# Optimization experiments

Measured on AMD Instinct MI355X. Metric: run time of the kernel, lower is better.

## Reference

```python
import jax, jax.numpy as jnp
import numpy as np

EMBED = 896
HQ = 16      # query heads
HK = 4       # kv heads
D = EMBED // HQ          # 56 head dim
KV_EMBED = D * HK        # 224
G = HQ // HK             # 4 groups per kv head
LN_EPS = 1e-5


def setup_inputs() -> dict:
    key = jax.random.key(0)
    ks = jax.random.split(key, 8)
    b, n = 2, 2048
    inp = {
        "query": jax.random.normal(ks[0], (b, n, EMBED), jnp.float32),
        "key":   jax.random.normal(ks[1], (b, n, EMBED), jnp.float32),
        "value": jax.random.normal(ks[2], (b, n, EMBED), jnp.float32),
        # torch Linear weights are (out_features, in_features), y = x @ W.T
        "Wq": jax.random.normal(ks[3], (EMBED, EMBED), jnp.float32) * 0.02,
        "Wk": jax.random.normal(ks[4], (KV_EMBED, EMBED), jnp.float32) * 0.02,
        "Wv": jax.random.normal(ks[5], (KV_EMBED, EMBED), jnp.float32) * 0.02,
        "Wo": jax.random.normal(ks[6], (EMBED, EMBED), jnp.float32) * 0.02,
        "ln_gamma": jnp.ones((EMBED,), jnp.float32),
        "ln_beta": jnp.zeros((EMBED,), jnp.float32),
    }
    return inp


def _layer_norm(x, gamma, beta):
    mu = jnp.mean(x, axis=-1, keepdims=True)
    var = jnp.var(x, axis=-1, keepdims=True)
    return (x - mu) * jax.lax.rsqrt(var + LN_EPS) * gamma + beta


def reference(query, key, value, Wq, Wk, Wv, Wo, ln_gamma, ln_beta):
    b, n, _ = query.shape
    s = key.shape[1]
    # projections
    q = query @ Wq.T                      # (b, n, EMBED)
    k = key @ Wk.T                        # (b, s, KV_EMBED)
    v = value @ Wv.T                      # (b, s, KV_EMBED)
    # split heads: q -> (b, hk, g, n, d); k, v -> (b, hk, s, d)
    q = q.reshape(b, n, HQ, D).transpose(0, 2, 1, 3)      # (b, hq, n, d)
    q = q.reshape(b, HK, G, n, D)                          # (b, hk, g, n, d)
    k = k.reshape(b, s, HK, D).transpose(0, 2, 1, 3)       # (b, hk, s, d)
    v = v.reshape(b, s, HK, D).transpose(0, 2, 1, 3)       # (b, hk, s, d)
    # scaled scores
    scale = jnp.asarray(D, q.dtype) ** 0.5
    scores = jnp.einsum('bhgnd,bhsd->bhgns', q, k) / scale  # (b, hk, g, n, s)
    # causal mask
    mask = jnp.tril(jnp.ones((n, s), bool))                # (n, s)
    scores = jnp.where(mask, scores, jnp.asarray(-jnp.inf, scores.dtype))
    attn = jax.nn.softmax(scores, axis=-1)                 # (b, hk, g, n, s)
    # (dropout is identity in deterministic eval-mode reference)
    out = jnp.einsum('bhgns,bhsd->bhgnd', attn, v)         # (b, hk, g, n, d)
    # merge heads back: (h g) ordering matches the query split
    out = out.transpose(0, 3, 1, 2, 4).reshape(b, n, EMBED)  # b n (h g d)
    out = _layer_norm(out, ln_gamma, ln_beta)
    out = out @ Wo.T                                        # (b, n, EMBED)
    # need_weights + average_attn_weights: b h g n s -> b n s (h g), mean over n
    aw = attn.transpose(0, 3, 4, 1, 2).reshape(b, n, s, HQ).mean(axis=1)  # (b, s, hq)
    return out, aw
```

## Files before the change

### kernel.cpp

```cpp
#include <hip/hip_runtime.h>

#define B_    2
#define N_    2048
#define EMBED 896
#define HQ    16
#define HK    4
#define D_    56
#define DP    64

typedef unsigned short u16;
typedef unsigned int   u32;
typedef __attribute__((ext_vector_type(8))) short bf16x8;
typedef __attribute__((ext_vector_type(4))) short bf16x4;
typedef __attribute__((ext_vector_type(4))) float f32x4;

__device__ __forceinline__ u16 f2bf(float f) {
  u32 u = __builtin_bit_cast(u32, f);
  return (u16)((u + 0x7FFFu + ((u >> 16) & 1u)) >> 16);
}

__device__ __forceinline__ float bf2f(u16 x) {
  u32 u = (u32)x << 16;
  return __builtin_bit_cast(float, u);
}

__device__ __forceinline__ u32 cvtpk_bf16(float lo, float hi) {
  u32 r;
  asm("v_cvt_pk_bf16_f32 %0, %1, %2" : "=v"(r) : "v"(lo), "v"(hi));
  return r;
}

#define EXP2F(x) __builtin_amdgcn_exp2f(x)

__device__ __forceinline__ void gload_lds16(const u16* g, u16* l) {
  __builtin_amdgcn_global_load_lds(
      (const __attribute__((address_space(1))) void*)g,
      (__attribute__((address_space(3))) void*)l, 16, 0, 0);
}

#define QSCALE 0.19278822f

__global__ __launch_bounds__(256) void pad_zero(u16* __restrict__ Qp,
                                                u16* __restrict__ Kp,
                                                u16* __restrict__ Vt) {
  int i = blockIdx.x * 256 + threadIdx.x;
  int4 z = {0, 0, 0, 0};
  if (i < 65536) {
    *(int4*)(Qp + (size_t)i * 64 + 56) = z;
  } else if (i < 81920) {
    *(int4*)(Kp + (size_t)(i - 65536) * 64 + 56) = z;
  } else {
    int j = i - 81920;
    int bhk = j >> 11;
    int off = j & 2047;
    *(int4*)(Vt + ((size_t)bhk * 64 + 56) * 2048 + (size_t)off * 8) = z;
  }
}

#define SEG_IN  3670016u
#define SEG_WQ  802816u
#define SEG_WK  200704u

__global__ __launch_bounds__(256) void to_bf16(
    const float* __restrict__ q, const float* __restrict__ k,
    const float* __restrict__ v, const float* __restrict__ wq,
    const float* __restrict__ wk, const float* __restrict__ wv,
    const float* __restrict__ wo, u16* __restrict__ qb, u16* __restrict__ kb,
    u16* __restrict__ vb, u16* __restrict__ wqb, u16* __restrict__ wkb,
    u16* __restrict__ wvb, u16* __restrict__ wob) {
  const size_t base = (size_t)blockIdx.x * 1024 + threadIdx.x;
  float4 v4[4];
  const float* srcs[4];
  u16* dsts[4];
  size_t offs[4];
#pragma unroll
  for (int j = 0; j < 4; j++) {
    size_t e = (base + j * 256) * 4;
    const float* src;
    u16* dst;
    size_t off;
    if (e < SEG_IN)                  { src = q;  dst = qb;  off = e; }
    else if (e < 2 * (size_t)SEG_IN) { src = k;  dst = kb;  off = e - SEG_IN; }
    else if (e < 3 * (size_t)SEG_IN) { src = v;  dst = vb;  off = e - 2 * (size_t)SEG_IN; }
    else {
      size_t r = e - 3 * (size_t)SEG_IN;
      if (r < SEG_WQ)                   { src = wq; dst = wqb; off = r; }
      else if (r < SEG_WQ + SEG_WK)     { src = wk; dst = wkb; off = r - SEG_WQ; }
      else if (r < SEG_WQ + 2 * SEG_WK) { src = wv; dst = wvb; off = r - SEG_WQ - SEG_WK; }
      else                              { src = wo; dst = wob; off = r - SEG_WQ - 2 * SEG_WK; }
    }
    srcs[j] = src; dsts[j] = dst; offs[j] = off;
    v4[j] = *(const float4*)(src + off);
  }
#pragma unroll
  for (int j = 0; j < 4; j++) {
    uint2 pb;
    pb.x = cvtpk_bf16(v4[j].x, v4[j].y);
    pb.y = cvtpk_bf16(v4[j].z, v4[j].w);
    *(uint2*)(dsts[j] + offs[j]) = pb;
  }
}

#define NT_K 14

#define GEMM_CORE(APTR, WPTR)                                                  \
  for (int it = 0; it < NT_K; ++it) {                                          \
    const int k0 = it * 64;                                                    \
    {                                                                          \
      const u16* Ag = (APTR) + (size_t)m0 * EMBED + k0;                        \
      _Pragma("unroll") for (int i = 0; i < 4; i++) {                          \
        int f = i * 256 + t;                                                   \
        int r = f >> 3, s = (f & 7) ^ (r & 7);                                 \
        gload_lds16(Ag + (size_t)r * EMBED + s * 8,                            \
                    AsL + (i * 256 + fwbase) * 8);                             \
      }                                                                        \
      const u16* Wg = (WPTR) + (size_t)wn0 * EMBED + k0;                       \
      _Pragma("unroll") for (int i = 0; i < 2; i++) {                          \
        int f = i * 256 + t;                                                   \
        int r = f >> 3, s = (f & 7) ^ (r & 7);                                 \
        gload_lds16(Wg + (size_t)r * EMBED + s * 8,                            \
                    BsL + (i * 256 + fwbase) * 8);                             \
      }                                                                        \
    }                                                                          \
    __syncthreads();                  \
    _Pragma("unroll") for (int kk = 0; kk < 2; kk++) {                         \
      bf16x8 af[2], bfv[4];                                                    \
      _Pragma("unroll") for (int mf = 0; mf < 2; mf++) {                       \
        int ra = wr + mf * 16 + fr;                                            \
        af[mf] =                                                               \
            *(const bf16x8*)&AsL[ra * 64 + ((fg + kk * 4) ^ (ra & 7)) * 8];    \
      }                                                                        \
      _Pragma("unroll") for (int nf = 0; nf < 4; nf++) {                       \
        int rb = nf * 16 + fr;                                                 \
        bfv[nf] =                                                              \
            *(const bf16x8*)&BsL[rb * 64 + ((fg + kk * 4) ^ (rb & 7)) * 8];    \
      }                                                                        \
      _Pragma("unroll") for (int mf = 0; mf < 2; mf++)                         \
          _Pragma("unroll") for (int nf = 0; nf < 4; nf++)                     \
              acc[mf][nf] = __builtin_amdgcn_mfma_f32_16x16x32_bf16(           \
                  af[mf], bfv[nf], acc[mf][nf], 0, 0, 0);                      \
    }                                                                          \
    __syncthreads();        \
  }

__global__ __launch_bounds__(256) void proj_gemm(
    const u16* __restrict__ qb, const u16* __restrict__ kb,
    const u16* __restrict__ vb, const u16* __restrict__ Wqb,
    const u16* __restrict__ Wkb, const u16* __restrict__ Wvb,
    u16* __restrict__ Qp, u16* __restrict__ Kp, u16* __restrict__ Vt) {
  __shared__ __align__(16) u16 lds[12288];
  u16* AsL = lds;
  u16* BsL = lds + 8192;
  const int t = threadIdx.x;
  const int bid = blockIdx.x;
  const int lin = (bid & 7) * 88 + (bid >> 3);
  const int y = lin / 32;
  const int m0 = (lin & 31) * 128;
  int p, nt;
  if (y < 14)      { p = 0; nt = y; }
  else if (y < 18) { p = 1; nt = y - 14; }
  else             { p = 2; nt = y - 18; }
  const u16* A = p == 0 ? qb : (p == 1 ? kb : vb);
  const u16* W = p == 0 ? Wqb : (p == 1 ? Wkb : Wvb);
  const int Nproj = p == 0 ? 896 : 224;
  const int wn0 = nt * 64;

  const int w = t >> 6, lane = t & 63;
  const int fr = lane & 15, fg = lane >> 4;
  const int wr = w * 32;
  const int fwbase = t & 192;

  f32x4 acc[2][4] = {};

  GEMM_CORE(A, W)

  if (p < 2) {
#pragma unroll
    for (int nf = 0; nf < 4; nf++) {
      int col = wn0 + nf * 16 + fr;
      if (col < Nproj) {
        int hh = col / 56, d = col - hh * 56;
#pragma unroll
        for (int mf = 0; mf < 2; mf++)
#pragma unroll
          for (int r = 0; r < 4; r++) {
            int row = m0 + wr + mf * 16 + fg * 4 + r;
            int bb = row >> 11, nn = row & 2047;
            float vv = acc[mf][nf][r];
            if (p == 0)
              Qp[((size_t)((bb * 16 + hh) * 2048 + nn)) * 64 + d] =
                  f2bf(vv * QSCALE);
            else
              Kp[((size_t)((bb * 4 + hh) * 2048 + nn)) * 64 + d] = f2bf(vv);
          }
      }
    }
  } else {
    u16* Traw = lds;
#define TS(r_, c_) Traw[(r_)*136 + (c_)]
#pragma unroll
    for (int nf = 0; nf < 4; nf++)
#pragma unroll
      for (int mf = 0; mf < 2; mf++)
#pragma unroll
        for (int r = 0; r < 4; r++)
          TS(nf * 16 + fr, wr + mf * 16 + fg * 4 + r) = f2bf(acc[mf][nf][r]);
    __syncthreads();
    const int bb = m0 >> 11, n_base = m0 & 2047;
#pragma unroll
    for (int i = 0; i < 4; i++) {
      int flat = i * 256 + t;
      int dr = flat >> 4;
      int c8 = (flat & 15) * 8;
      int col = wn0 + dr;
      if (col < 224) {
        int hh = col / 56, d = col - hh * 56;
        *(int4*)(Vt + ((size_t)((bb * 4 + hh) * 64 + d)) * 2048 + n_base + c8) =
            *(int4*)&TS(dr, c8);
      }
    }
  }
}

__global__ __launch_bounds__(256) void gemm_wo(const u16* __restrict__ A,
                                               const u16* __restrict__ W,
                                               float* __restrict__ C) {
  __shared__ __align__(16) u16 lds[12288];
  u16* AsL = lds;
  u16* BsL = lds + 8192;
  const int t = threadIdx.x;
  const int m0 = blockIdx.x * 128;
  const int wn0 = blockIdx.y * 64;
  const int w = t >> 6, lane = t & 63;
  const int fr = lane & 15, fg = lane >> 4;
  const int wr = w * 32;
  const int fwbase = t & 192;

  f32x4 acc[2][4] = {};

  GEMM_CORE(A, W)

#pragma unroll
  for (int nf = 0; nf < 4; nf++) {
    int col = wn0 + nf * 16 + fr;
#pragma unroll
    for (int mf = 0; mf < 2; mf++)
#pragma unroll
      for (int r = 0; r < 4; r++) {
        int row = m0 + wr + mf * 16 + fg * 4 + r;
        C[(size_t)row * EMBED + col] = acc[mf][nf][r];
      }
  }
}

__global__ __launch_bounds__(256) void repack_qf(const u16* __restrict__ Qp,
                                                 u16* __restrict__ Qf) {
  const int tile = blockIdx.x;
  const u16* src = Qp + (size_t)tile * 4096;
  u16* dst = Qf + (size_t)tile * 4096;
  __shared__ __align__(16) u16 T[4096];
  const int t = threadIdx.x;
#pragma unroll
  for (int i = 0; i < 2; i++) {
    int f = i * 256 + t;
    int r = f >> 3, c8 = f & 7;
    *(int4*)&T[(r * 8 + (c8 ^ (r & 7))) * 8] = *(const int4*)(src + f * 8);
  }
  __syncthreads();
#pragma unroll
  for (int i = 0; i < 2; i++) {
    int f = i * 256 + t;
    int fr = f & 15, fg = (f >> 4) & 3, kk = (f >> 6) & 1, ifr = (f >> 7) & 3;
    int row = ifr * 16 + fr, c8 = (kk * 32 + fg * 8) >> 3;
    *(int4*)(dst + f * 8) = *(int4*)&T[(row * 8 + (c8 ^ (row & 7))) * 8];
  }
}

__global__ __launch_bounds__(256) void attn_fwd(const u16* __restrict__ Qp,
                                                const u16* __restrict__ Kp,
                                                const u16* __restrict__ Vt,
                                                u16* __restrict__ Op,
                                                float* __restrict__ lp) {
  const int p = blockIdx.x, hk = blockIdx.y;
  const int b = blockIdx.z >> 1, sg = blockIdx.z & 1;
  const int t = threadIdx.x, w = t >> 6, lane = t & 63;
  const int fr = lane & 15, fg = lane >> 4;
  const int h = hk * 4 + w;

  __shared__ __align__(16) u16 KVs[2][2][4096];

  const u16* Qh = Qp + (size_t)(b * HQ + h) * N_ * DP;
  const u16* Kh = Kp + (size_t)(b * HK + hk) * N_ * DP;
  const u16* Vh = Vt + (size_t)(b * HK + hk) * DP * N_;

  const int fwb = t & 192;
  const int fx = fr & 7;

#define ISSUE_KV(ntt_, buf_)                                                   \
  do {                                                                         \
    const u16* Kb = Kh + (size_t)(ntt_)*64 * DP;                               \
    const u16* Vb = Vh + (ntt_)*64;                                            \
    _Pragma("unroll") for (int i = 0; i < 2; i++) {                            \
      int f = i * 256 + t;                                                     \
      int r = f >> 3, sl = (f & 7) ^ (r & 7);                                  \
      gload_lds16(Kb + (size_t)r * DP + sl * 8,                                \
                  &KVs[buf_][0][(i * 256 + fwb) * 8]);                         \
      gload_lds16(Vb + (size_t)r * N_ + sl * 8,                                \
                  &KVs[buf_][1][(i * 256 + fwb) * 8]);                         \
    }                                                                          \
  } while (0)

  const int s0 = p, s1 = 127 - p;
  const int ntf0 = (s0 >> 2) + 1, ntf1 = (s1 >> 2) + 1;
  const int lo0 = sg ? (ntf0 >> 1) : 0, hi0 = sg ? ntf0 : (ntf0 >> 1);
  const int lo1 = sg ? (ntf1 >> 1) : 0, hi1 = sg ? ntf1 : (ntf1 >> 1);

  int bi = 0;
  if (hi0 > lo0) {
    ISSUE_KV(lo0, 0);
  } else if (hi1 > lo1) {
    ISSUE_KV(lo1, 0);
  }

  for (int half = 0; half < 2; ++half) {
    const int s = half ? s1 : s0;
    const int ntf = half ? ntf1 : ntf0;
    const int lo = half ? lo1 : lo0, hi = half ? hi1 : hi0;

    bf16x8 qf[2];
#pragma unroll
    for (int kk = 0; kk < 2; kk++)
      qf[kk] = *(const bf16x8*)(Qh + (size_t)(s * 16 + fr) * DP +
                                kk * 32 + fg * 8);

    f32x4 oacc[4] = {};
    float l_lane = 0.f;

    for (int tt = lo; tt < hi; ++tt) {
      __syncthreads();
      {
        int ntt = -1;
        if (tt + 1 < hi) ntt = tt + 1;
        else if (half == 0 && hi1 > lo1) ntt = lo1;
        if (ntt >= 0) {
          ISSUE_KV(ntt, bi ^ 1);
        }
      }

      f32x4 sacc[4] = {};
#pragma unroll
      for (int kk = 0; kk < 2; kk++) {
        bf16x8 bk[4];
#pragma unroll
        for (int jf = 0; jf < 4; jf++)
          bk[jf] = *(const bf16x8*)&KVs[bi][0][(jf * 16 + fr) * 64 +
                                               ((kk * 4 + fg) ^ fx) * 8];
#pragma unroll
        for (int jf = 0; jf < 4; jf++)
          sacc[jf] = __builtin_amdgcn_mfma_f32_16x16x32_bf16(
              bk[jf], qf[kk], sacc[jf], 0, 0, 0);
      }

      bf16x4 pa[4];
      if (tt == ntf - 1) {
        const int gi = s * 16 + fr;
#pragma unroll
        for (int jf = 0; jf < 4; jf++) {
          float pv[4];
#pragma unroll
          for (int r = 0; r < 4; r++) {
            int gj = tt * 64 + jf * 16 + fg * 4 + r;
            pv[r] = (gj <= gi) ? EXP2F(sacc[jf][r]) : 0.f;
            l_lane += pv[r];
          }
          uint2 pk = {cvtpk_bf16(pv[0], pv[1]), cvtpk_bf16(pv[2], pv[3])};
          pa[jf] = __builtin_bit_cast(bf16x4, pk);
        }
      } else {
#pragma unroll
        for (int jf = 0; jf < 4; jf++) {
          float pv[4];
#pragma unroll
          for (int r = 0; r < 4; r++) {
            pv[r] = EXP2F(sacc[jf][r]);
            l_lane += pv[r];
          }
          uint2 pk = {cvtpk_bf16(pv[0], pv[1]), cvtpk_bf16(pv[2], pv[3])};
          pa[jf] = __builtin_bit_cast(bf16x4, pk);
        }
      }

#pragma unroll
      for (int df = 0; df < 4; df++) {
        const int vrow = (df * 16 + fr) * 64;
#pragma unroll
        for (int jf = 0; jf < 4; jf++) {
          bf16x4 bv = *(const bf16x4*)&KVs[bi][1][vrow +
                                                  (((jf * 2 + (fg >> 1)) ^ fx) * 8) +
                                                  (fg & 1) * 4];
          oacc[df] = __builtin_amdgcn_mfma_f32_16x16x16bf16_1k(
              pa[jf], bv, oacc[df], 0, 0, 0);
        }
      }
      bi ^= 1;
    }

    {
      float v = l_lane;
      v += __shfl_xor(v, 16);
      v += __shfl_xor(v, 32);
      const size_t obase = (((size_t)(sg * 2 + b) * 16 + h) * 2048 + s * 16);
      if (fg == 0) lp[obase + fr] = v;
#pragma unroll
      for (int df = 0; df < 4; df++) {
        int d = df * 16 + fr;
        if (d < D_) {
#pragma unroll
          for (int r = 0; r < 4; r++)
            Op[(obase + fg * 4 + r) * 56 + d] = f2bf(oacc[df][r]);
        }
      }
    }
    l_lane = 0.f;
  }
}

struct QTile {
  bf16x8 q[4][2];
  float li[4];
};

#define LOADQ(dst, rt_)                                                        \
  {                                                                            \
    _Pragma("unroll") for (int ifr = 0; ifr < 4; ifr++) {                      \
      _Pragma("unroll") for (int kk = 0; kk < 2; kk++)                         \
          dst.q[ifr][kk] = *(const bf16x8*)(Qfh +                              \
              ((((size_t)(rt_)*4 + ifr) * 2 + kk) * 64 + fg * 16 + fr) * 8);   \
      dst.li[ifr] = linv_h[(rt_)*64 + ifr * 16 + fr];                          \
    }                                                                          \
  }

#define COMPUTET(src, rt_)                                                     \
  {                                                                            \
    f32x4 tacc[2][4] = {};                                                     \
    _Pragma("unroll") for (int kk = 0; kk < 2; kk++)                           \
        _Pragma("unroll") for (int jm = 0; jm < 2; jm++)                       \
        _Pragma("unroll") for (int ifr = 0; ifr < 4; ifr++)                    \
            tacc[jm][ifr] = __builtin_amdgcn_mfma_f32_16x16x32_bf16(           \
                kf[jm][kk], src.q[ifr][kk], tacc[jm][ifr], 0, 0, 0);           \
    if ((rt_) == rt0) {                                                        \
      _Pragma("unroll") for (int jm = 0; jm < 2; jm++)                         \
          _Pragma("unroll") for (int ifr = 0; ifr < 4; ifr++)                  \
          _Pragma("unroll") for (int r = 0; r < 4; r++) {                      \
        int gi = (rt_)*64 + ifr * 16 + fr;                                     \
        int gj = ct * 32 + jm * 16 + fg * 4 + r;                               \
        if (gi >= gj)                                                          \
          s_acc[jm][r] += EXP2F(tacc[jm][ifr][r]) * src.li[ifr];               \
      }                                                                        \
    } else {                                                                   \
      _Pragma("unroll") for (int jm = 0; jm < 2; jm++)                         \
          _Pragma("unroll") for (int ifr = 0; ifr < 4; ifr++)                  \
          _Pragma("unroll") for (int r = 0; r < 4; r++)                        \
              s_acc[jm][r] += EXP2F(tacc[jm][ifr][r]) * src.li[ifr];           \
    }                                                                          \
  }

__global__ __launch_bounds__(256) void attn_aw(const u16* __restrict__ Qf,
                                               const u16* __restrict__ Kp,
                                               const float* __restrict__ linv_g,
                                               float* __restrict__ aw) {
  const int bid = blockIdx.x;
  const int xcd = bid & 7, idx = bid >> 3;
  const int g = xcd + 8 * (idx >> 5);
  const int p = idx & 31;
  const int b = g >> 4, h = g & 15;
  const int hk = h >> 2;
  const int t = threadIdx.x, w = t >> 6, lane = t & 63;
  const int fr = lane & 15, fg = lane >> 4;

  __shared__ float red[2][4][32];

  const u16* Qfh = Qf + (size_t)(b * HQ + h) * N_ * DP;
  const u16* Kh = Kp + (size_t)(b * HK + hk) * N_ * DP;
  const float* linv_h = linv_g + (size_t)(b * HQ + h) * N_;

  for (int half = 0; half < 2; ++half) {
    const int ct = half ? (63 - p) : p;
    const int rt0 = ct >> 1;

    bf16x8 kf[2][2];
#pragma unroll
    for (int jm = 0; jm < 2; jm++)
#pragma unroll
      for (int kk = 0; kk < 2; kk++)
        kf[jm][kk] = *(const bf16x8*)(Kh + (size_t)(ct * 32 + jm * 16 + fr) * DP +
                                      kk * 32 + fg * 8);

    float s_acc[2][4] = {};
    QTile qa, qb;
    int rt = rt0 + w;
    if (rt <= 31) {
      LOADQ(qa, rt);
      while (true) {
        if (rt + 4 <= 31) LOADQ(qb, rt + 4);
        COMPUTET(qa, rt);
        rt += 4;
        if (rt > 31) break;
        if (rt + 4 <= 31) LOADQ(qa, rt + 4);
        COMPUTET(qb, rt);
        rt += 4;
        if (rt > 31) break;
      }
    }

#pragma unroll
    for (int jm = 0; jm < 2; jm++)
#pragma unroll
      for (int r = 0; r < 4; r++) {
        float v = s_acc[jm][r];
        v += __shfl_xor(v, 1);
        v += __shfl_xor(v, 2);
        v += __shfl_xor(v, 4);
        v += __shfl_xor(v, 8);
        if (fr == 0) red[half][w][jm * 16 + fg * 4 + r] = v;
      }
  }

  __syncthreads();
  if (w == 0 && fr == 0) {
#pragma unroll
    for (int half = 0; half < 2; ++half) {
      const int ct = half ? (63 - p) : p;
#pragma unroll
      for (int jm = 0; jm < 2; jm++)
#pragma unroll
        for (int r = 0; r < 4; r++) {
          int idx2 = jm * 16 + fg * 4 + r;
          float v = red[half][0][idx2] + red[half][1][idx2] +
                    red[half][2][idx2] + red[half][3][idx2];
          int gj = ct * 32 + jm * 16 + fg * 4 + r;
          aw[((size_t)b * N_ + gj) * HQ + h] = v * (1.0f / N_);
        }
    }
  }
}

__global__ __launch_bounds__(256) void ln_fwd(const u16* __restrict__ Op,
                                              const float* __restrict__ lp,
                                              const float* __restrict__ gamma,
                                              const float* __restrict__ beta,
                                              u16* __restrict__ out,
                                              float* __restrict__ linv_g) {
  const int row = blockIdx.x;
  const int b = row >> 11, n = row & 2047;
  const int t = threadIdx.x;
  __shared__ float lrec[16];
  __shared__ float red[8];

  if (t < 16) {
    float l0 = lp[((size_t)(0 + b) * 16 + t) * 2048 + n];
    float l1 = lp[((size_t)(2 + b) * 16 + t) * 2048 + n];
    float ri = 1.0f / (l0 + l1);
    lrec[t] = ri;
    linv_g[((size_t)b * 16 + t) * 2048 + n] = ri;
  }
  __syncthreads();

  float s = 0.f, s2 = 0.f;
  float v[4];
#pragma unroll
  for (int i = 0; i < 4; i++) {
    int c = t + 256 * i;
    if (c < EMBED) {
      int h = c / 56, d = c - h * 56;
      size_t o0 = (((size_t)(0 + b) * 16 + h) * 2048 + n) * 56 + d;
      size_t o1 = (((size_t)(2 + b) * 16 + h) * 2048 + n) * 56 + d;
      v[i] = (bf2f(Op[o0]) + bf2f(Op[o1])) * lrec[h];
    } else {
      v[i] = 0.f;
    }
    s += v[i];
    s2 += v[i] * v[i];
  }
#pragma unroll
  for (int m = 1; m <= 32; m <<= 1) {
    s += __shfl_xor(s, m);
    s2 += __shfl_xor(s2, m);
  }
  const int w = t >> 6, lane = t & 63;
  if (lane == 0) {
    red[w] = s;
    red[4 + w] = s2;
  }
  __syncthreads();
  s = red[0] + red[1] + red[2] + red[3];
  s2 = red[4] + red[5] + red[6] + red[7];
  const float mu = s * (1.0f / EMBED);
  const float var = s2 * (1.0f / EMBED) - mu * mu;
  const float rs = rsqrtf(var + 1e-5f);
#pragma unroll
  for (int i = 0; i < 4; i++) {
    int c = t + 256 * i;
    if (c < EMBED)
      out[(size_t)row * EMBED + c] = f2bf((v[i] - mu) * rs * gamma[c] + beta[c]);
  }
}

extern "C" void kernel_launch(void* const* d_in, const int* in_sizes, int n_in,
                              void* d_out, int out_size, void* d_ws,
                              size_t ws_size, hipStream_t stream) {
  (void)in_sizes; (void)n_in; (void)out_size; (void)ws_size;
  const float* query = (const float*)d_in[0];
  const float* key   = (const float*)d_in[1];
  const float* value = (const float*)d_in[2];
  const float* Wq    = (const float*)d_in[3];
  const float* Wk    = (const float*)d_in[4];
  const float* Wv    = (const float*)d_in[5];
  const float* Wo    = (const float*)d_in[6];
  const float* gamma = (const float*)d_in[7];
  const float* beta  = (const float*)d_in[8];

  float* out = (float*)d_out;
  float* aw  = out + (size_t)B_ * N_ * EMBED;

  char* ws = (char*)d_ws;
  u16* Qp = (u16*)ws;        ws += (size_t)B_ * HQ * N_ * DP * 2;
  u16* Kp = (u16*)ws;        ws += (size_t)B_ * HK * N_ * DP * 2;
  u16* Vt = (u16*)ws;        ws += (size_t)B_ * HK * N_ * DP * 2;
  u16* Qf = (u16*)ws;        ws += (size_t)B_ * HQ * N_ * DP * 2;
  float* linv = (float*)ws;  ws += (size_t)B_ * HQ * N_ * 4;
  float* lp   = (float*)ws;  ws += (size_t)4 * HQ * N_ * 4;
  u16* Wqb = (u16*)ws;       ws += (size_t)SEG_WQ * 2;
  u16* Wkb = (u16*)ws;       ws += (size_t)SEG_WK * 2;
  u16* Wvb = (u16*)ws;       ws += (size_t)SEG_WK * 2;
  u16* Wob = (u16*)ws;       ws += (size_t)SEG_WQ * 2;
  char* region = ws;
  u16* qb = (u16*)region;
  u16* kb = qb + (size_t)SEG_IN;
  u16* vb = kb + (size_t)SEG_IN;
  u16* Op  = (u16*)region;
  u16* LNo = Op + (size_t)4 * HQ * N_ * 56;

  dim3 blk(256);
  const int M = B_ * N_;

  pad_zero<<<dim3(384), blk, 0, stream>>>(Qp, Kp, Vt);

  to_bf16<<<dim3(3178), blk, 0, stream>>>(query, key, value, Wq, Wk, Wv, Wo,
                                          qb, kb, vb, Wqb, Wkb, Wvb, Wob);

  proj_gemm<<<dim3(704), blk, 0, stream>>>(qb, kb, vb, Wqb, Wkb, Wvb,
                                           Qp, Kp, Vt);

  repack_qf<<<dim3(B_ * HQ * (N_ / 64)), blk, 0, stream>>>(Qp, Qf);

  attn_fwd<<<dim3(64, HK, B_ * 2), blk, 0, stream>>>(Qp, Kp, Vt, Op, lp);
  ln_fwd<<<dim3(M), blk, 0, stream>>>(Op, lp, gamma, beta, LNo, linv);

  attn_aw<<<dim3(1024), blk, 0, stream>>>(Qf, Kp, linv, aw);
  gemm_wo<<<dim3(M / 128, 14), blk, 0, stream>>>(LNo, Wob, out);
}
```

Measured before the change: 122.6 us.

## Write Q directly in fragment layout from projection GEMM and drop repack kernel

The Q projection epilogue now scatters results straight into the MFMA-fragment tiled layout (Qf) that the attention kernels consume, and attn_fwd reads from that layout. This removes the separate repack_qf kernel and its extra write and read of Q. The padding kernel is updated to zero the pad slots in the new layout. Separately, gemm_wo switches to a 1D grid with an XCD-aware block remap for cache locality. The scattered 2-byte stores in the Q epilogue are less coalesced than before.

```diff
diff --git a/kernel.cpp b/kernel.cpp
--- a/kernel.cpp
+++ b/kernel.cpp
@@ -40,13 +40,15 @@
 
 #define QSCALE 0.19278822f
 
-__global__ __launch_bounds__(256) void pad_zero(u16* __restrict__ Qp,
+__global__ __launch_bounds__(256) void pad_zero(u16* __restrict__ Qf,
                                                 u16* __restrict__ Kp,
                                                 u16* __restrict__ Vt) {
   int i = blockIdx.x * 256 + threadIdx.x;
   int4 z = {0, 0, 0, 0};
   if (i < 65536) {
-    *(int4*)(Qp + (size_t)i * 64 + 56) = z;
+    int tile = i >> 6, ifr = (i >> 4) & 3, fr = i & 15;
+    *(int4*)(Qf + (size_t)tile * 4096 +
+             ((((ifr * 2 + 1) * 4 + 3) * 16) + fr) * 8) = z;
   } else if (i < 81920) {
     *(int4*)(Kp + (size_t)(i - 65536) * 64 + 56) = z;
   } else {
@@ -70,7 +72,6 @@
     u16* __restrict__ wvb, u16* __restrict__ wob) {
   const size_t base = (size_t)blockIdx.x * 1024 + threadIdx.x;
   float4 v4[4];
-  const float* srcs[4];
   u16* dsts[4];
   size_t offs[4];
 #pragma unroll
@@ -89,7 +90,7 @@
       else if (r < SEG_WQ + 2 * SEG_WK) { src = wv; dst = wvb; off = r - SEG_WQ - SEG_WK; }
       else                              { src = wo; dst = wob; off = r - SEG_WQ - 2 * SEG_WK; }
     }
-    srcs[j] = src; dsts[j] = dst; offs[j] = off;
+    dsts[j] = dst; offs[j] = off;
     v4[j] = *(const float4*)(src + off);
   }
 #pragma unroll
@@ -147,7 +148,7 @@
     const u16* __restrict__ qb, const u16* __restrict__ kb,
     const u16* __restrict__ vb, const u16* __restrict__ Wqb,
     const u16* __restrict__ Wkb, const u16* __restrict__ Wvb,
-    u16* __restrict__ Qp, u16* __restrict__ Kp, u16* __restrict__ Vt) {
+    u16* __restrict__ Qf, u16* __restrict__ Kp, u16* __restrict__ Vt) {
   __shared__ __align__(16) u16 lds[12288];
   u16* AsL = lds;
   u16* BsL = lds + 8192;
@@ -174,7 +175,26 @@
 
   GEMM_CORE(A, W)
 
-  if (p < 2) {
+  if (p == 0) {
+#pragma unroll
+    for (int nf = 0; nf < 4; nf++) {
+      int col = wn0 + nf * 16 + fr;
+      int hh = col / 56, d = col - hh * 56;
+      int kkq = d >> 5, fgq = (d & 31) >> 3, c7 = d & 7;
+#pragma unroll
+      for (int mf = 0; mf < 2; mf++)
+#pragma unroll
+        for (int r = 0; r < 4; r++) {
+          int row = m0 + wr + mf * 16 + fg * 4 + r;
+          int bb = row >> 11, nn = row & 2047;
+          int tile = (bb * 16 + hh) * 32 + (nn >> 6);
+          int irow = nn & 63, ifr = irow >> 4, frq = irow & 15;
+          Qf[(size_t)tile * 4096 +
+             ((((ifr * 2 + kkq) * 4 + fgq) * 16) + frq) * 8 + c7] =
+              f2bf(acc[mf][nf][r] * QSCALE);
+        }
+    }
+  } else if (p == 1) {
 #pragma unroll
     for (int nf = 0; nf < 4; nf++) {
       int col = wn0 + nf * 16 + fr;
@@ -186,12 +206,8 @@
           for (int r = 0; r < 4; r++) {
             int row = m0 + wr + mf * 16 + fg * 4 + r;
             int bb = row >> 11, nn = row & 2047;
-            float vv = acc[mf][nf][r];
-            if (p == 0)
-              Qp[((size_t)((bb * 16 + hh) * 2048 + nn)) * 64 + d] =
-                  f2bf(vv * QSCALE);
-            else
-              Kp[((size_t)((bb * 4 + hh) * 2048 + nn)) * 64 + d] = f2bf(vv);
+            Kp[((size_t)((bb * 4 + hh) * 2048 + nn)) * 64 + d] =
+                f2bf(acc[mf][nf][r]);
           }
       }
     }
@@ -229,8 +245,10 @@
   u16* AsL = lds;
   u16* BsL = lds + 8192;
   const int t = threadIdx.x;
-  const int m0 = blockIdx.x * 128;
-  const int wn0 = blockIdx.y * 64;
+  const int bid = blockIdx.x;
+  const int lin = (bid & 7) * 56 + (bid >> 3);
+  const int m0 = (lin & 31) * 128;
+  const int wn0 = (lin >> 5) * 64;
   const int w = t >> 6, lane = t & 63;
   const int fr = lane & 15, fg = lane >> 4;
   const int wr = w * 32;
@@ -253,30 +271,7 @@
   }
 }
 
-__global__ __launch_bounds__(256) void repack_qf(const u16* __restrict__ Qp,
-                                                 u16* __restrict__ Qf) {
-  const int tile = blockIdx.x;
-  const u16* src = Qp + (size_t)tile * 4096;
-  u16* dst = Qf + (size_t)tile * 4096;
-  __shared__ __align__(16) u16 T[4096];
-  const int t = threadIdx.x;
-#pragma unroll
-  for (int i = 0; i < 2; i++) {
-    int f = i * 256 + t;
-    int r = f >> 3, c8 = f & 7;
-    *(int4*)&T[(r * 8 + (c8 ^ (r & 7))) * 8] = *(const int4*)(src + f * 8);
-  }
-  __syncthreads();
-#pragma unroll
-  for (int i = 0; i < 2; i++) {
-    int f = i * 256 + t;
-    int fr = f & 15, fg = (f >> 4) & 3, kk = (f >> 6) & 1, ifr = (f >> 7) & 3;
-    int row = ifr * 16 + fr, c8 = (kk * 32 + fg * 8) >> 3;
-    *(int4*)(dst + f * 8) = *(int4*)&T[(row * 8 + (c8 ^ (row & 7))) * 8];
-  }
-}
-
-__global__ __launch_bounds__(256) void attn_fwd(const u16* __restrict__ Qp,
+__global__ __launch_bounds__(256) void attn_fwd(const u16* __restrict__ Qf,
                                                 const u16* __restrict__ Kp,
                                                 const u16* __restrict__ Vt,
                                                 u16* __restrict__ Op,
@@ -289,7 +284,7 @@
 
   __shared__ __align__(16) u16 KVs[2][2][4096];
 
-  const u16* Qh = Qp + (size_t)(b * HQ + h) * N_ * DP;
+  const u16* Qfh = Qf + (size_t)(b * HQ + h) * N_ * DP;
   const u16* Kh = Kp + (size_t)(b * HK + hk) * N_ * DP;
   const u16* Vh = Vt + (size_t)(b * HK + hk) * DP * N_;
 
@@ -330,8 +325,9 @@
     bf16x8 qf[2];
 #pragma unroll
     for (int kk = 0; kk < 2; kk++)
-      qf[kk] = *(const bf16x8*)(Qh + (size_t)(s * 16 + fr) * DP +
-                                kk * 32 + fg * 8);
+      qf[kk] = *(const bf16x8*)(Qfh + ((size_t)(s >> 2) * 512 +
+                                       ((s & 3) * 2 + kk) * 64 +
+                                       fg * 16 + fr) * 8);
 
     f32x4 oacc[4] = {};
     float l_lane = 0.f;
@@ -624,10 +620,9 @@
   float* aw  = out + (size_t)B_ * N_ * EMBED;
 
   char* ws = (char*)d_ws;
-  u16* Qp = (u16*)ws;        ws += (size_t)B_ * HQ * N_ * DP * 2;
+  u16* Qf = (u16*)ws;        ws += (size_t)B_ * HQ * N_ * DP * 2;
   u16* Kp = (u16*)ws;        ws += (size_t)B_ * HK * N_ * DP * 2;
   u16* Vt = (u16*)ws;        ws += (size_t)B_ * HK * N_ * DP * 2;
-  u16* Qf = (u16*)ws;        ws += (size_t)B_ * HQ * N_ * DP * 2;
   float* linv = (float*)ws;  ws += (size_t)B_ * HQ * N_ * 4;
   float* lp   = (float*)ws;  ws += (size_t)4 * HQ * N_ * 4;
   u16* Wqb = (u16*)ws;       ws += (size_t)SEG_WQ * 2;
@@ -644,19 +639,17 @@
   dim3 blk(256);
   const int M = B_ * N_;
 
-  pad_zero<<<dim3(384), blk, 0, stream>>>(Qp, Kp, Vt);
+  pad_zero<<<dim3(384), blk, 0, stream>>>(Qf, Kp, Vt);
 
   to_bf16<<<dim3(3178), blk, 0, stream>>>(query, key, value, Wq, Wk, Wv, Wo,
                                           qb, kb, vb, Wqb, Wkb, Wvb, Wob);
 
   proj_gemm<<<dim3(704), blk, 0, stream>>>(qb, kb, vb, Wqb, Wkb, Wvb,
-                                           Qp, Kp, Vt);
-
-  repack_qf<<<dim3(B_ * HQ * (N_ / 64)), blk, 0, stream>>>(Qp, Qf);
-
-  attn_fwd<<<dim3(64, HK, B_ * 2), blk, 0, stream>>>(Qp, Kp, Vt, Op, lp);
+                                           Qf, Kp, Vt);
+
+  attn_fwd<<<dim3(64, HK, B_ * 2), blk, 0, stream>>>(Qf, Kp, Vt, Op, lp);
   ln_fwd<<<dim3(M), blk, 0, stream>>>(Op, lp, gamma, beta, LNo, linv);
 
   attn_aw<<<dim3(1024), blk, 0, stream>>>(Qf, Kp, linv, aw);
-  gemm_wo<<<dim3(M / 128, 14), blk, 0, stream>>>(LNo, Wob, out);
-}
+  gemm_wo<<<dim3(448), blk, 0, stream>>>(LNo, Wob, out);
+}
```

Measured after the change: 120.3 us. Within noise of the previous version (-1.8%).
